# Performance work log

Measured on AMD Instinct MI355X. Metric: run time of the kernel, lower is better.

## Reference

```python
import jax, jax.numpy as jnp
import numpy as np

PI = float(np.pi)

def erp_xyz_coords(h, w):
    # matches calculate_erp_coord: pixel grid -> uv -> unit-sphere xyz
    yy, xx = jnp.meshgrid(jnp.linspace(0.0, h - 1.0, h), jnp.linspace(0.0, w - 1.0, w), indexing='ij')
    u = (xx - (w / 2.0 + 0.5)) / w * 2.0 * PI
    v = (yy - (h / 2.0 + 0.5)) / h * PI
    xyz = jnp.stack([jnp.cos(v) * jnp.sin(u), jnp.sin(v), jnp.cos(v) * jnp.cos(u)], axis=-1)
    return xyz.reshape(h * w, 3)  # (HW, 3)


def setup_inputs() -> dict:
    key = jax.random.key(0)
    ks = jax.random.split(key, 16)
    B, C, H, W = 1, 128, 16, 32
    Nkv = 1280
    s = 0.02
    inp = {
        'erp_feature': jax.random.normal(ks[0], (B, C, H, W), jnp.float32),
        'ico_feature': jax.random.normal(ks[1], (B, Nkv, C), jnp.float32),
        'ico_coord': jax.random.normal(ks[2], (B, Nkv, 3), jnp.float32),
        # SA branch params (torch Linear: y = x @ W.T + b, W is (out,in))
        'Wq_sa': jax.random.normal(ks[3], (C, C), jnp.float32) * s,
        'Wkv_sa': jax.random.normal(ks[4], (2 * C, C), jnp.float32) * s,
        'proj_sa_w': jax.random.normal(ks[5], (C, C), jnp.float32) * s,
        'proj_sa_b': jnp.zeros((C,), jnp.float32),
        # DA branch params
        'Wq_da': jax.random.normal(ks[6], (C, C), jnp.float32) * s,
        'Wkv_da': jax.random.normal(ks[7], (2 * C, C), jnp.float32) * s,
        'Wdelta': jax.random.normal(ks[8], (C, 3), jnp.float32) * s,
        'proj_da_w': jax.random.normal(ks[9], (C, C), jnp.float32) * s,
        'proj_da_b': jnp.zeros((C,), jnp.float32),
        # gates
        'gate_sa_w': jax.random.normal(ks[10], (C, 2 * C), jnp.float32) * s,
        'gate_da_w': jax.random.normal(ks[11], (C, 2 * C), jnp.float32) * s,
    }
    return inp


def _forward(erp_feature, ico_feature, ico_coord,
             Wq_sa, Wkv_sa, proj_sa_w, proj_sa_b,
             Wq_da, Wkv_da, Wdelta, proj_da_w, proj_da_b,
             gate_sa_w, gate_da_w):
    B, C, H, W = erp_feature.shape
    Nq = H * W
    q = erp_feature.reshape(B, C, Nq).transpose(0, 2, 1)  # (B, Nq, C)
    qc = erp_xyz_coords(H, W)[None]                        # (1, Nq, 3) broadcasts over B

    # ---- SA branch (iteration = 1) ----
    q_sa = q @ Wq_sa.T                                     # (B, Nq, C)
    kv_sa = (ico_feature @ Wkv_sa.T).reshape(B, -1, 2, C)
    k_sa, v_sa = kv_sa[:, :, 0], kv_sa[:, :, 1]
    attn_sa = jax.nn.softmax(jnp.einsum('bqc,bkc->bqk', q_sa, k_sa) * (C ** -0.5), axis=-1)
    out_sa = jnp.einsum('bqk,bkc->bqc', attn_sa, v_sa)
    # faithful to torch: .transpose(1,2).reshape(B, Nq, C) scrambles layout
    out_sa = out_sa.transpose(0, 2, 1).reshape(B, Nq, C)
    sa = out_sa @ proj_sa_w.T + proj_sa_b

    # ---- DA branch (iteration = 1) ----
    q_da = q @ Wq_da.T
    kv_da = (ico_feature @ Wkv_da.T).reshape(B, -1, 2, C)
    k_da, v_da = kv_da[:, :, 0], kv_da[:, :, 1]
    # feature affinity: sum_c exp(-|q_c - k_c|)   -> (B, Nq, Nkv)
    feat_aff = jnp.exp(-jnp.abs(q_da[:, :, None, :] - k_da[:, None, :, :])).sum(-1)
    # positional term: (exp(-|dq - dk|) @ Wdelta.T).sum(-1) == exp(...) . Wdelta.sum(0)
    pos_exp = jnp.exp(-jnp.abs(qc[:, :, None, :] - ico_coord[:, None, :, :]))  # (B,Nq,Nkv,3)
    pos_aff = jnp.einsum('bqkt,t->bqk', pos_exp, Wdelta.sum(0))
    attn_da = jax.nn.softmax((feat_aff + pos_aff) * (1.0 / C), axis=-1)
    out_da = jnp.einsum('bqk,bkc->bqc', attn_da, v_da)
    da = out_da @ proj_da_w.T + proj_da_b

    # ---- gated fusion ----
    cat = jnp.concatenate([sa, da], axis=-1)               # (B, Nq, 2C)
    sa_factor = jax.nn.sigmoid(cat @ gate_sa_w.T)
    da_factor = jax.nn.sigmoid(cat @ gate_da_w.T)
    fused = sa_factor * sa + da_factor * da                # (B, Nq, C)
    return fused.reshape(B, H, W, C).transpose(0, 3, 1, 2)  # (B, C, H, W)


def reference(erp_feature, ico_feature, ico_coord,
              Wq_sa, Wkv_sa, proj_sa_w, proj_sa_b,
              Wq_da, Wkv_da, Wdelta, proj_da_w, proj_da_b,
              gate_sa_w, gate_da_w):
    return _forward(erp_feature, ico_feature, ico_coord,
                    Wq_sa, Wkv_sa, proj_sa_w, proj_sa_b,
                    Wq_da, Wkv_da, Wdelta, proj_da_w, proj_da_b,
                    gate_sa_w, gate_da_w)
```

## Files before the change

### kernel.cpp

```cpp
#include <hip/hip_runtime.h>
#include <math.h>

#define NQ   512
#define NKV  1280
#define CDIM 128

#define OFF_WDSUM  0
#define OFF_QSA    16
#define OFF_QDA    65552
#define OFF_KSAT   131088
#define OFF_VSA    294928
#define OFF_KDAT   458768
#define OFF_VDA    622608
#define OFF_OUTSA  786448
#define OFF_OUTDA  851984
#define OFF_LOG_SA 917520
#define OFF_LOG_DA 1572880

__global__ __launch_bounds__(256) void proj_kernel(
    const float* __restrict__ erp, const float* __restrict__ ico,
    const float* __restrict__ wq_sa, const float* __restrict__ wq_da,
    const float* __restrict__ wkv_sa, const float* __restrict__ wkv_da,
    const float* __restrict__ wdelta, float* __restrict__ ws)
{
  int bx = blockIdx.x, t = threadIdx.x;
  if (bx < 128) {
    __shared__ float q4[4 * CDIM];
    int n0 = bx * 4;
    for (int i = t; i < 512; i += 256)
      q4[i] = erp[(i >> 2) * NQ + n0 + (i & 3)];
    __syncthreads();
    const float* w = (t < 128) ? wq_sa : wq_da;
    int c = t & 127;
    const float4* w4 = (const float4*)(w + c * CDIM);
    float a0 = 0.f, a1 = 0.f, a2 = 0.f, a3 = 0.f;
    #pragma unroll 8
    for (int j4 = 0; j4 < 32; ++j4) {
      float4 wv = w4[j4];
      float4 q0 = *(const float4*)&q4[(j4 * 4 + 0) * 4];
      float4 q1 = *(const float4*)&q4[(j4 * 4 + 1) * 4];
      float4 q2 = *(const float4*)&q4[(j4 * 4 + 2) * 4];
      float4 q3 = *(const float4*)&q4[(j4 * 4 + 3) * 4];
      a0 = fmaf(wv.x, q0.x, a0); a1 = fmaf(wv.x, q0.y, a1);
      a2 = fmaf(wv.x, q0.z, a2); a3 = fmaf(wv.x, q0.w, a3);
      a0 = fmaf(wv.y, q1.x, a0); a1 = fmaf(wv.y, q1.y, a1);
      a2 = fmaf(wv.y, q1.z, a2); a3 = fmaf(wv.y, q1.w, a3);
      a0 = fmaf(wv.z, q2.x, a0); a1 = fmaf(wv.z, q2.y, a1);
      a2 = fmaf(wv.z, q2.z, a2); a3 = fmaf(wv.z, q2.w, a3);
      a0 = fmaf(wv.w, q3.x, a0); a1 = fmaf(wv.w, q3.y, a1);
      a2 = fmaf(wv.w, q3.z, a2); a3 = fmaf(wv.w, q3.w, a3);
    }
    float* o = ws + ((t < 128) ? OFF_QSA : OFF_QDA);
    o[(n0 + 0) * CDIM + c] = a0;
    o[(n0 + 1) * CDIM + c] = a1;
    o[(n0 + 2) * CDIM + c] = a2;
    o[(n0 + 3) * CDIM + c] = a3;
  } else if (bx < 448) {
    __shared__ float x4[4 * CDIM];
    int k0 = (bx - 128) * 4;
    for (int i = t; i < 512; i += 256) {
      int ky = i >> 7, j = i & 127;
      x4[j * 4 + ky] = ico[(k0 + ky) * CDIM + j];
    }
    __syncthreads();
    const float4* wsa4 = (const float4*)(wkv_sa + t * CDIM);
    const float4* wda4 = (const float4*)(wkv_da + t * CDIM);
    float as0=0,as1=0,as2=0,as3=0, ad0=0,ad1=0,ad2=0,ad3=0;
    #pragma unroll 4
    for (int j4 = 0; j4 < 32; ++j4) {
      float4 wsv = wsa4[j4];
      float4 wdv = wda4[j4];
      float4 x0 = *(const float4*)&x4[(j4 * 4 + 0) * 4];
      float4 x1 = *(const float4*)&x4[(j4 * 4 + 1) * 4];
      float4 x2 = *(const float4*)&x4[(j4 * 4 + 2) * 4];
      float4 x3 = *(const float4*)&x4[(j4 * 4 + 3) * 4];
      as0 = fmaf(wsv.x, x0.x, as0); as1 = fmaf(wsv.x, x0.y, as1);
      as2 = fmaf(wsv.x, x0.z, as2); as3 = fmaf(wsv.x, x0.w, as3);
      ad0 = fmaf(wdv.x, x0.x, ad0); ad1 = fmaf(wdv.x, x0.y, ad1);
      ad2 = fmaf(wdv.x, x0.z, ad2); ad3 = fmaf(wdv.x, x0.w, ad3);
      as0 = fmaf(wsv.y, x1.x, as0); as1 = fmaf(wsv.y, x1.y, as1);
      as2 = fmaf(wsv.y, x1.z, as2); as3 = fmaf(wsv.y, x1.w, as3);
      ad0 = fmaf(wdv.y, x1.x, ad0); ad1 = fmaf(wdv.y, x1.y, ad1);
      ad2 = fmaf(wdv.y, x1.z, ad2); ad3 = fmaf(wdv.y, x1.w, ad3);
      as0 = fmaf(wsv.z, x2.x, as0); as1 = fmaf(wsv.z, x2.y, as1);
      as2 = fmaf(wsv.z, x2.z, as2); as3 = fmaf(wsv.z, x2.w, as3);
      ad0 = fmaf(wdv.z, x2.x, ad0); ad1 = fmaf(wdv.z, x2.y, ad1);
      ad2 = fmaf(wdv.z, x2.z, ad2); ad3 = fmaf(wdv.z, x2.w, ad3);
      as0 = fmaf(wsv.w, x3.x, as0); as1 = fmaf(wsv.w, x3.y, as1);
      as2 = fmaf(wsv.w, x3.z, as2); as3 = fmaf(wsv.w, x3.w, as3);
      ad0 = fmaf(wdv.w, x3.x, ad0); ad1 = fmaf(wdv.w, x3.y, ad1);
      ad2 = fmaf(wdv.w, x3.z, ad2); ad3 = fmaf(wdv.w, x3.w, ad3);
    }
    if (t < 128) {
      *(float4*)(ws + OFF_KSAT + t * NKV + k0) = make_float4(as0, as1, as2, as3);
      *(float4*)(ws + OFF_KDAT + t * NKV + k0) = make_float4(ad0, ad1, ad2, ad3);
    } else {
      int c = t - 128;
      ws[OFF_VSA + (k0 + 0) * CDIM + c] = as0;
      ws[OFF_VSA + (k0 + 1) * CDIM + c] = as1;
      ws[OFF_VSA + (k0 + 2) * CDIM + c] = as2;
      ws[OFF_VSA + (k0 + 3) * CDIM + c] = as3;
      ws[OFF_VDA + (k0 + 0) * CDIM + c] = ad0;
      ws[OFF_VDA + (k0 + 1) * CDIM + c] = ad1;
      ws[OFF_VDA + (k0 + 2) * CDIM + c] = ad2;
      ws[OFF_VDA + (k0 + 3) * CDIM + c] = ad3;
    }
  } else {
    __shared__ float acc[3];
    if (t < 3) acc[t] = 0.f;
    __syncthreads();
    if (t < 128) {
      atomicAdd(&acc[0], wdelta[t * 3 + 0]);
      atomicAdd(&acc[1], wdelta[t * 3 + 1]);
      atomicAdd(&acc[2], wdelta[t * 3 + 2]);
    }
    __syncthreads();
    if (t < 3) ws[OFF_WDSUM + t] = acc[t];
  }
}

__global__ __launch_bounds__(256) void score_kernel(
    const float* __restrict__ coord, float* __restrict__ ws)
{
  __shared__ float4 q4[CDIM];
  __shared__ float qcr[4][3];
  __shared__ float wd[3];
  int t = threadIdx.x;
  int n0 = blockIdx.x * 4;
  int br = blockIdx.y;
  int k  = blockIdx.z * 256 + t;
  float* qf = (float*)q4;
  const float* qsrc = ws + (br ? OFF_QDA : OFF_QSA);
  for (int i = t; i < 4 * CDIM; i += 256) {
    int r = i >> 7, j = i & 127;
    qf[j * 4 + r] = qsrc[(n0 + r) * CDIM + j];
  }
  if (br && t < 4) {
    int n = n0 + t;
    float x = (float)(n & 31), y = (float)(n >> 5);
    float u  = (x - 16.5f) * 0.19634954084936207f;
    float vv = (y -  8.5f) * 0.19634954084936207f;
    float cv = cosf(vv);
    qcr[t][0] = cv * sinf(u);
    qcr[t][1] = sinf(vv);
    qcr[t][2] = cv * cosf(u);
  }
  if (br && t < 3) wd[t] = ws[OFF_WDSUM + t];
  __syncthreads();

  if (br == 0) {
    const float* ksat = ws + OFF_KSAT;
    float a0 = 0.f, a1 = 0.f, a2 = 0.f, a3 = 0.f;
    #pragma unroll 8
    for (int j = 0; j < CDIM; ++j) {
      float kv = ksat[j * NKV + k];
      float4 q = q4[j];
      a0 = fmaf(q.x, kv, a0);
      a1 = fmaf(q.y, kv, a1);
      a2 = fmaf(q.z, kv, a2);
      a3 = fmaf(q.w, kv, a3);
    }
    const float scale = 0.088388347648318447f;
    float* lg = ws + OFF_LOG_SA;
    lg[(n0 + 0) * NKV + k] = a0 * scale;
    lg[(n0 + 1) * NKV + k] = a1 * scale;
    lg[(n0 + 2) * NKV + k] = a2 * scale;
    lg[(n0 + 3) * NKV + k] = a3 * scale;
  } else {
    float c0 = coord[k * 3], c1 = coord[k * 3 + 1], c2 = coord[k * 3 + 2];
    const float* kdat = ws + OFF_KDAT;
    float a0 = 0.f, a1 = 0.f, a2 = 0.f, a3 = 0.f;
    #pragma unroll 8
    for (int j = 0; j < CDIM; ++j) {
      float kv = kdat[j * NKV + k];
      float4 q = q4[j];
      a0 += __expf(-fabsf(q.x - kv));
      a1 += __expf(-fabsf(q.y - kv));
      a2 += __expf(-fabsf(q.z - kv));
      a3 += __expf(-fabsf(q.w - kv));
    }
    float w0 = wd[0], w1 = wd[1], w2 = wd[2];
    float* lg = ws + OFF_LOG_DA;
    #pragma unroll
    for (int r = 0; r < 4; ++r) {
      float p = w0 * __expf(-fabsf(qcr[r][0] - c0))
              + w1 * __expf(-fabsf(qcr[r][1] - c1))
              + w2 * __expf(-fabsf(qcr[r][2] - c2));
      float a = (r == 0) ? a0 : (r == 1) ? a1 : (r == 2) ? a2 : a3;
      lg[(n0 + r) * NKV + k] = (a + p) * 0.0078125f;
    }
  }
}

__global__ __launch_bounds__(256) void softmax_av_kernel(float* __restrict__ ws)
{
  __shared__ float sc[2][NKV];
  __shared__ float red[8];
  __shared__ float part[4][2][CDIM];
  int t = threadIdx.x;
  int n0 = blockIdx.x * 2;
  int br = blockIdx.y;
  const float* lg = ws + (br ? OFF_LOG_DA : OFF_LOG_SA);
  float v0[5], v1[5];
  float lm0 = -1e30f, lm1 = -1e30f;
  #pragma unroll
  for (int ki = 0; ki < 5; ++ki) {
    v0[ki] = lg[(n0 + 0) * NKV + ki * 256 + t];
    v1[ki] = lg[(n0 + 1) * NKV + ki * 256 + t];
    lm0 = fmaxf(lm0, v0[ki]);
    lm1 = fmaxf(lm1, v1[ki]);
  }
  for (int o = 32; o > 0; o >>= 1) {
    lm0 = fmaxf(lm0, __shfl_down(lm0, o, 64));
    lm1 = fmaxf(lm1, __shfl_down(lm1, o, 64));
  }
  if ((t & 63) == 0) { red[t >> 6] = lm0; red[4 + (t >> 6)] = lm1; }
  __syncthreads();
  float m0 = fmaxf(fmaxf(red[0], red[1]), fmaxf(red[2], red[3]));
  float m1 = fmaxf(fmaxf(red[4], red[5]), fmaxf(red[6], red[7]));
  float s0 = 0.f, s1 = 0.f;
  #pragma unroll
  for (int ki = 0; ki < 5; ++ki) {
    float e0 = __expf(v0[ki] - m0);
    float e1 = __expf(v1[ki] - m1);
    sc[0][ki * 256 + t] = e0;
    sc[1][ki * 256 + t] = e1;
    s0 += e0; s1 += e1;
  }
  for (int o = 32; o > 0; o >>= 1) {
    s0 += __shfl_down(s0, o, 64);
    s1 += __shfl_down(s1, o, 64);
  }
  __syncthreads();
  if ((t & 63) == 0) { red[t >> 6] = s0; red[4 + (t >> 6)] = s1; }
  __syncthreads();
  float is0 = 1.0f / (red[0] + red[1] + red[2] + red[3]);
  float is1 = 1.0f / (red[4] + red[5] + red[6] + red[7]);

  const float* v = ws + (br ? OFF_VDA : OFF_VSA);
  int quarter = t >> 6;
  int c0 = (t & 63) * 2;
  int kb = quarter * 320;
  float a00 = 0.f, a01 = 0.f, a10 = 0.f, a11 = 0.f;
  #pragma unroll 2
  for (int ko = 0; ko < 320; ko += 4) {
    int k = kb + ko;
    float4 p0 = *(const float4*)&sc[0][k];
    float4 p1 = *(const float4*)&sc[1][k];
    float2 va = *(const float2*)&v[(k + 0) * CDIM + c0];
    float2 vb = *(const float2*)&v[(k + 1) * CDIM + c0];
    float2 vc = *(const float2*)&v[(k + 2) * CDIM + c0];
    float2 vd = *(const float2*)&v[(k + 3) * CDIM + c0];
    a00 = fmaf(p0.x, va.x, a00); a01 = fmaf(p0.x, va.y, a01);
    a10 = fmaf(p1.x, va.x, a10); a11 = fmaf(p1.x, va.y, a11);
    a00 = fmaf(p0.y, vb.x, a00); a01 = fmaf(p0.y, vb.y, a01);
    a10 = fmaf(p1.y, vb.x, a10); a11 = fmaf(p1.y, vb.y, a11);
    a00 = fmaf(p0.z, vc.x, a00); a01 = fmaf(p0.z, vc.y, a01);
    a10 = fmaf(p1.z, vc.x, a10); a11 = fmaf(p1.z, vc.y, a11);
    a00 = fmaf(p0.w, vd.x, a00); a01 = fmaf(p0.w, vd.y, a01);
    a10 = fmaf(p1.w, vd.x, a10); a11 = fmaf(p1.w, vd.y, a11);
  }
  part[quarter][0][c0] = a00; part[quarter][0][c0 + 1] = a01;
  part[quarter][1][c0] = a10; part[quarter][1][c0 + 1] = a11;
  __syncthreads();
  {
    int r = t >> 7, c = t & 127;
    float sum = part[0][r][c] + part[1][r][c] + part[2][r][c] + part[3][r][c];
    float* o = ws + (br ? OFF_OUTDA : OFF_OUTSA);
    o[(n0 + r) * CDIM + c] = sum * (r ? is1 : is0);
  }
}

__global__ __launch_bounds__(128) void finalize_kernel(
    const float* __restrict__ psa, const float* __restrict__ bsa,
    const float* __restrict__ pda, const float* __restrict__ bda,
    const float* __restrict__ gsa, const float* __restrict__ gda,
    float* __restrict__ out, float* __restrict__ ws)
{
  __shared__ float sain[CDIM];
  __shared__ float dain[CDIM];
  __shared__ float cat[2 * CDIM];
  int i = blockIdx.x, t = threadIdx.x;
  sain[t] = ws[OFF_OUTSA + ((i & 3) * 128 + t) * CDIM + (i >> 2)];
  dain[t] = ws[OFF_OUTDA + i * CDIM + t];
  __syncthreads();
  const float4* p4 = (const float4*)(psa + t * CDIM);
  const float4* d4 = (const float4*)(pda + t * CDIM);
  float s0=0,s1=0,s2=0,s3=0, e0=0,e1=0,e2=0,e3=0;
  #pragma unroll 8
  for (int j4 = 0; j4 < 32; ++j4) {
    float4 wv = p4[j4];
    float4 xv = *(const float4*)&sain[j4 * 4];
    s0 = fmaf(wv.x, xv.x, s0); s1 = fmaf(wv.y, xv.y, s1);
    s2 = fmaf(wv.z, xv.z, s2); s3 = fmaf(wv.w, xv.w, s3);
    float4 wv2 = d4[j4];
    float4 yv = *(const float4*)&dain[j4 * 4];
    e0 = fmaf(wv2.x, yv.x, e0); e1 = fmaf(wv2.y, yv.y, e1);
    e2 = fmaf(wv2.z, yv.z, e2); e3 = fmaf(wv2.w, yv.w, e3);
  }
  float asa = bsa[t] + ((s0 + s1) + (s2 + s3));
  float ada = bda[t] + ((e0 + e1) + (e2 + e3));
  cat[t] = asa;
  cat[CDIM + t] = ada;
  __syncthreads();
  const float4* g14 = (const float4*)(gsa + t * 2 * CDIM);
  const float4* g24 = (const float4*)(gda + t * 2 * CDIM);
  float u0=0,u1=0,u2=0,u3=0, w0=0,w1=0,w2=0,w3=0;
  #pragma unroll 8
  for (int j4 = 0; j4 < 64; ++j4) {
    float4 gv = g14[j4];
    float4 cv = *(const float4*)&cat[j4 * 4];
    u0 = fmaf(gv.x, cv.x, u0); u1 = fmaf(gv.y, cv.y, u1);
    u2 = fmaf(gv.z, cv.z, u2); u3 = fmaf(gv.w, cv.w, u3);
    float4 gv2 = g24[j4];
    w0 = fmaf(gv2.x, cv.x, w0); w1 = fmaf(gv2.y, cv.y, w1);
    w2 = fmaf(gv2.z, cv.z, w2); w3 = fmaf(gv2.w, cv.w, w3);
  }
  float g1 = 1.0f / (1.0f + __expf(-((u0 + u1) + (u2 + u3))));
  float g2 = 1.0f / (1.0f + __expf(-((w0 + w1) + (w2 + w3))));
  out[t * NQ + i] = g1 * asa + g2 * ada;
}

extern "C" void kernel_launch(void* const* d_in, const int* in_sizes, int n_in,
                              void* d_out, int out_size, void* d_ws, size_t ws_size,
                              hipStream_t stream)
{
  (void)in_sizes; (void)n_in; (void)out_size; (void)ws_size;
  const float* erp       = (const float*)d_in[0];
  const float* ico       = (const float*)d_in[1];
  const float* coord     = (const float*)d_in[2];
  const float* wq_sa     = (const float*)d_in[3];
  const float* wkv_sa    = (const float*)d_in[4];
  const float* proj_sa_w = (const float*)d_in[5];
  const float* proj_sa_b = (const float*)d_in[6];
  const float* wq_da     = (const float*)d_in[7];
  const float* wkv_da    = (const float*)d_in[8];
  const float* wdelta    = (const float*)d_in[9];
  const float* proj_da_w = (const float*)d_in[10];
  const float* proj_da_b = (const float*)d_in[11];
  const float* gate_sa   = (const float*)d_in[12];
  const float* gate_da   = (const float*)d_in[13];
  float* out = (float*)d_out;
  float* ws  = (float*)d_ws;

  hipLaunchKernelGGL(proj_kernel, dim3(449), dim3(256), 0, stream,
                     erp, ico, wq_sa, wq_da, wkv_sa, wkv_da, wdelta, ws);
  hipLaunchKernelGGL(score_kernel, dim3(128, 2, 5), dim3(256), 0, stream,
                     coord, ws);
  hipLaunchKernelGGL(softmax_av_kernel, dim3(256, 2), dim3(256), 0, stream, ws);
  hipLaunchKernelGGL(finalize_kernel, dim3(512), dim3(128), 0, stream,
                     proj_sa_w, proj_sa_b, proj_da_w, proj_da_b,
                     gate_sa, gate_da, out, ws);
}
```

Before: 173.4 us.

## Fuse Q projection and score computation into the softmax-AV attention kernel

Removes the separate score kernel and the Q-projection part of the projection kernel. Each attention block now computes its two query rows' projections in shared memory, computes all 1280 logits per row in registers, and goes straight into softmax and AV. This drops the global logit buffers and a kernel launch, but only 512 blocks now compute scores, each doing 2 rows instead of 4, so K reads are reused less.

```diff
diff --git a/kernel.cpp b/kernel.cpp
--- a/kernel.cpp
+++ b/kernel.cpp
@@ -6,58 +6,22 @@
 #define CDIM 128
 
 #define OFF_WDSUM  0
-#define OFF_QSA    16
-#define OFF_QDA    65552
-#define OFF_KSAT   131088
-#define OFF_VSA    294928
-#define OFF_KDAT   458768
-#define OFF_VDA    622608
-#define OFF_OUTSA  786448
-#define OFF_OUTDA  851984
-#define OFF_LOG_SA 917520
-#define OFF_LOG_DA 1572880
-
-__global__ __launch_bounds__(256) void proj_kernel(
-    const float* __restrict__ erp, const float* __restrict__ ico,
-    const float* __restrict__ wq_sa, const float* __restrict__ wq_da,
+#define OFF_KSAT   16
+#define OFF_VSA    163856
+#define OFF_KDAT   327696
+#define OFF_VDA    491536
+#define OFF_OUTSA  655376
+#define OFF_OUTDA  720912
+
+__global__ __launch_bounds__(256) void kvproj_kernel(
+    const float* __restrict__ ico,
     const float* __restrict__ wkv_sa, const float* __restrict__ wkv_da,
     const float* __restrict__ wdelta, float* __restrict__ ws)
 {
   int bx = blockIdx.x, t = threadIdx.x;
-  if (bx < 128) {
-    __shared__ float q4[4 * CDIM];
-    int n0 = bx * 4;
-    for (int i = t; i < 512; i += 256)
-      q4[i] = erp[(i >> 2) * NQ + n0 + (i & 3)];
-    __syncthreads();
-    const float* w = (t < 128) ? wq_sa : wq_da;
-    int c = t & 127;
-    const float4* w4 = (const float4*)(w + c * CDIM);
-    float a0 = 0.f, a1 = 0.f, a2 = 0.f, a3 = 0.f;
-    #pragma unroll 8
-    for (int j4 = 0; j4 < 32; ++j4) {
-      float4 wv = w4[j4];
-      float4 q0 = *(const float4*)&q4[(j4 * 4 + 0) * 4];
-      float4 q1 = *(const float4*)&q4[(j4 * 4 + 1) * 4];
-      float4 q2 = *(const float4*)&q4[(j4 * 4 + 2) * 4];
-      float4 q3 = *(const float4*)&q4[(j4 * 4 + 3) * 4];
-      a0 = fmaf(wv.x, q0.x, a0); a1 = fmaf(wv.x, q0.y, a1);
-      a2 = fmaf(wv.x, q0.z, a2); a3 = fmaf(wv.x, q0.w, a3);
-      a0 = fmaf(wv.y, q1.x, a0); a1 = fmaf(wv.y, q1.y, a1);
-      a2 = fmaf(wv.y, q1.z, a2); a3 = fmaf(wv.y, q1.w, a3);
-      a0 = fmaf(wv.z, q2.x, a0); a1 = fmaf(wv.z, q2.y, a1);
-      a2 = fmaf(wv.z, q2.z, a2); a3 = fmaf(wv.z, q2.w, a3);
-      a0 = fmaf(wv.w, q3.x, a0); a1 = fmaf(wv.w, q3.y, a1);
-      a2 = fmaf(wv.w, q3.z, a2); a3 = fmaf(wv.w, q3.w, a3);
-    }
-    float* o = ws + ((t < 128) ? OFF_QSA : OFF_QDA);
-    o[(n0 + 0) * CDIM + c] = a0;
-    o[(n0 + 1) * CDIM + c] = a1;
-    o[(n0 + 2) * CDIM + c] = a2;
-    o[(n0 + 3) * CDIM + c] = a3;
-  } else if (bx < 448) {
+  if (bx < 320) {
     __shared__ float x4[4 * CDIM];
-    int k0 = (bx - 128) * 4;
+    int k0 = bx * 4;
     for (int i = t; i < 512; i += 256) {
       int ky = i >> 7, j = i & 127;
       x4[j * 4 + ky] = ico[(k0 + ky) * CDIM + j];
@@ -119,96 +83,111 @@
   }
 }
 
-__global__ __launch_bounds__(256) void score_kernel(
-    const float* __restrict__ coord, float* __restrict__ ws)
+__global__ __launch_bounds__(256) void attn_kernel(
+    const float* __restrict__ erp, const float* __restrict__ coord,
+    const float* __restrict__ wq_sa, const float* __restrict__ wq_da,
+    float* __restrict__ ws)
 {
-  __shared__ float4 q4[CDIM];
-  __shared__ float qcr[4][3];
-  __shared__ float wd[3];
-  int t = threadIdx.x;
-  int n0 = blockIdx.x * 4;
-  int br = blockIdx.y;
-  int k  = blockIdx.z * 256 + t;
-  float* qf = (float*)q4;
-  const float* qsrc = ws + (br ? OFF_QDA : OFF_QSA);
-  for (int i = t; i < 4 * CDIM; i += 256) {
-    int r = i >> 7, j = i & 127;
-    qf[j * 4 + r] = qsrc[(n0 + r) * CDIM + j];
-  }
-  if (br && t < 4) {
-    int n = n0 + t;
-    float x = (float)(n & 31), y = (float)(n >> 5);
-    float u  = (x - 16.5f) * 0.19634954084936207f;
-    float vv = (y -  8.5f) * 0.19634954084936207f;
-    float cv = cosf(vv);
-    qcr[t][0] = cv * sinf(u);
-    qcr[t][1] = sinf(vv);
-    qcr[t][2] = cv * cosf(u);
-  }
-  if (br && t < 3) wd[t] = ws[OFF_WDSUM + t];
-  __syncthreads();
-
-  if (br == 0) {
-    const float* ksat = ws + OFF_KSAT;
-    float a0 = 0.f, a1 = 0.f, a2 = 0.f, a3 = 0.f;
-    #pragma unroll 8
-    for (int j = 0; j < CDIM; ++j) {
-      float kv = ksat[j * NKV + k];
-      float4 q = q4[j];
-      a0 = fmaf(q.x, kv, a0);
-      a1 = fmaf(q.y, kv, a1);
-      a2 = fmaf(q.z, kv, a2);
-      a3 = fmaf(q.w, kv, a3);
-    }
-    const float scale = 0.088388347648318447f;
-    float* lg = ws + OFF_LOG_SA;
-    lg[(n0 + 0) * NKV + k] = a0 * scale;
-    lg[(n0 + 1) * NKV + k] = a1 * scale;
-    lg[(n0 + 2) * NKV + k] = a2 * scale;
-    lg[(n0 + 3) * NKV + k] = a3 * scale;
-  } else {
-    float c0 = coord[k * 3], c1 = coord[k * 3 + 1], c2 = coord[k * 3 + 2];
-    const float* kdat = ws + OFF_KDAT;
-    float a0 = 0.f, a1 = 0.f, a2 = 0.f, a3 = 0.f;
-    #pragma unroll 8
-    for (int j = 0; j < CDIM; ++j) {
-      float kv = kdat[j * NKV + k];
-      float4 q = q4[j];
-      a0 += __expf(-fabsf(q.x - kv));
-      a1 += __expf(-fabsf(q.y - kv));
-      a2 += __expf(-fabsf(q.z - kv));
-      a3 += __expf(-fabsf(q.w - kv));
-    }
-    float w0 = wd[0], w1 = wd[1], w2 = wd[2];
-    float* lg = ws + OFF_LOG_DA;
-    #pragma unroll
-    for (int r = 0; r < 4; ++r) {
-      float p = w0 * __expf(-fabsf(qcr[r][0] - c0))
-              + w1 * __expf(-fabsf(qcr[r][1] - c1))
-              + w2 * __expf(-fabsf(qcr[r][2] - c2));
-      float a = (r == 0) ? a0 : (r == 1) ? a1 : (r == 2) ? a2 : a3;
-      lg[(n0 + r) * NKV + k] = (a + p) * 0.0078125f;
-    }
-  }
-}
-
-__global__ __launch_bounds__(256) void softmax_av_kernel(float* __restrict__ ws)
-{
+  __shared__ float eq[2][CDIM];
+  __shared__ float q2[CDIM * 2];
   __shared__ float sc[2][NKV];
   __shared__ float red[8];
   __shared__ float part[4][2][CDIM];
+  __shared__ float qcr[2][3];
+  __shared__ float wd[3];
   int t = threadIdx.x;
   int n0 = blockIdx.x * 2;
   int br = blockIdx.y;
-  const float* lg = ws + (br ? OFF_LOG_DA : OFF_LOG_SA);
-  float v0[5], v1[5];
+
+  {
+    int r = t >> 7, j = t & 127;
+    eq[r][j] = erp[j * NQ + n0 + r];
+  }
+  if (br) {
+    if (t < 2) {
+      int n = n0 + t;
+      float x = (float)(n & 31), y = (float)(n >> 5);
+      float u  = (x - 16.5f) * 0.19634954084936207f;
+      float vv = (y -  8.5f) * 0.19634954084936207f;
+      float cv = cosf(vv);
+      qcr[t][0] = cv * sinf(u);
+      qcr[t][1] = sinf(vv);
+      qcr[t][2] = cv * cosf(u);
+    }
+    if (t >= 64 && t < 67) wd[t - 64] = ws[OFF_WDSUM + t - 64];
+  }
+  __syncthreads();
+
+  {
+    int r = t >> 7, c = t & 127;
+    const float* w = br ? wq_da : wq_sa;
+    const float4* w4 = (const float4*)(w + c * CDIM);
+    const float4* x4 = (const float4*)eq[r];
+    float a0 = 0.f, a1 = 0.f, a2 = 0.f, a3 = 0.f;
+    #pragma unroll 8
+    for (int j4 = 0; j4 < 32; ++j4) {
+      float4 wv = w4[j4];
+      float4 xv = x4[j4];
+      a0 = fmaf(wv.x, xv.x, a0); a1 = fmaf(wv.y, xv.y, a1);
+      a2 = fmaf(wv.z, xv.z, a2); a3 = fmaf(wv.w, xv.w, a3);
+    }
+    q2[c * 2 + r] = (a0 + a1) + (a2 + a3);
+  }
+  __syncthreads();
+
+  float l0[5], l1[5];
+  if (br == 0) {
+    const float* K = ws + OFF_KSAT + t;
+    float a0[5] = {0,0,0,0,0}, a1[5] = {0,0,0,0,0};
+    #pragma unroll 4
+    for (int j = 0; j < CDIM; ++j) {
+      float2 q = *(const float2*)&q2[j * 2];
+      const float* kj = K + j * NKV;
+      #pragma unroll
+      for (int ki = 0; ki < 5; ++ki) {
+        float kv = kj[ki * 256];
+        a0[ki] = fmaf(q.x, kv, a0[ki]);
+        a1[ki] = fmaf(q.y, kv, a1[ki]);
+      }
+    }
+    const float scale = 0.088388347648318447f;
+    #pragma unroll
+    for (int ki = 0; ki < 5; ++ki) { l0[ki] = a0[ki] * scale; l1[ki] = a1[ki] * scale; }
+  } else {
+    const float* K = ws + OFF_KDAT + t;
+    float a0[5] = {0,0,0,0,0}, a1[5] = {0,0,0,0,0};
+    #pragma unroll 2
+    for (int j = 0; j < CDIM; ++j) {
+      float2 q = *(const float2*)&q2[j * 2];
+      const float* kj = K + j * NKV;
+      #pragma unroll
+      for (int ki = 0; ki < 5; ++ki) {
+        float kv = kj[ki * 256];
+        a0[ki] += __expf(-fabsf(q.x - kv));
+        a1[ki] += __expf(-fabsf(q.y - kv));
+      }
+    }
+    float w0 = wd[0], w1 = wd[1], w2 = wd[2];
+    float q00 = qcr[0][0], q01 = qcr[0][1], q02 = qcr[0][2];
+    float q10 = qcr[1][0], q11 = qcr[1][1], q12 = qcr[1][2];
+    #pragma unroll
+    for (int ki = 0; ki < 5; ++ki) {
+      int k = t + ki * 256;
+      float c0 = coord[k * 3], c1 = coord[k * 3 + 1], c2 = coord[k * 3 + 2];
+      float p0 = w0 * __expf(-fabsf(q00 - c0)) + w1 * __expf(-fabsf(q01 - c1))
+               + w2 * __expf(-fabsf(q02 - c2));
+      float p1 = w0 * __expf(-fabsf(q10 - c0)) + w1 * __expf(-fabsf(q11 - c1))
+               + w2 * __expf(-fabsf(q12 - c2));
+      l0[ki] = (a0[ki] + p0) * 0.0078125f;
+      l1[ki] = (a1[ki] + p1) * 0.0078125f;
+    }
+  }
+
   float lm0 = -1e30f, lm1 = -1e30f;
   #pragma unroll
   for (int ki = 0; ki < 5; ++ki) {
-    v0[ki] = lg[(n0 + 0) * NKV + ki * 256 + t];
-    v1[ki] = lg[(n0 + 1) * NKV + ki * 256 + t];
-    lm0 = fmaxf(lm0, v0[ki]);
-    lm1 = fmaxf(lm1, v1[ki]);
+    lm0 = fmaxf(lm0, l0[ki]);
+    lm1 = fmaxf(lm1, l1[ki]);
   }
   for (int o = 32; o > 0; o >>= 1) {
     lm0 = fmaxf(lm0, __shfl_down(lm0, o, 64));
@@ -221,8 +200,8 @@
   float s0 = 0.f, s1 = 0.f;
   #pragma unroll
   for (int ki = 0; ki < 5; ++ki) {
-    float e0 = __expf(v0[ki] - m0);
-    float e1 = __expf(v1[ki] - m1);
+    float e0 = __expf(l0[ki] - m0);
+    float e1 = __expf(l1[ki] - m1);
     sc[0][ki * 256 + t] = e0;
     sc[1][ki * 256 + t] = e1;
     s0 += e0; s1 += e1;
@@ -343,11 +322,10 @@
   float* out = (float*)d_out;
   float* ws  = (float*)d_ws;
 
-  hipLaunchKernelGGL(proj_kernel, dim3(449), dim3(256), 0, stream,
-                     erp, ico, wq_sa, wq_da, wkv_sa, wkv_da, wdelta, ws);
-  hipLaunchKernelGGL(score_kernel, dim3(128, 2, 5), dim3(256), 0, stream,
-                     coord, ws);
-  hipLaunchKernelGGL(softmax_av_kernel, dim3(256, 2), dim3(256), 0, stream, ws);
+  hipLaunchKernelGGL(kvproj_kernel, dim3(321), dim3(256), 0, stream,
+                     ico, wkv_sa, wkv_da, wdelta, ws);
+  hipLaunchKernelGGL(attn_kernel, dim3(256, 2), dim3(256), 0, stream,
+                     erp, coord, wq_sa, wq_da, ws);
   hipLaunchKernelGGL(finalize_kernel, dim3(512), dim3(128), 0, stream,
                      proj_sa_w, proj_sa_b, proj_da_w, proj_da_b,
                      gate_sa, gate_da, out, ws);
```

New measurement: 180.6 us. 1.04x slower.
